# Optimization experiments

Measured on AMD Instinct MI355X. Metric: run time of the kernel, lower is better.

The kernel has to match this reference:

```python
import jax, jax.numpy as jnp
import numpy as np

EPS = 1e-5
BATCH = 2
VOX_H = 8  # grid resolution at depth - stages = 3


def conv_bn_relu(x, neigh, W, gamma, beta):
    # octree sparse conv: gather 27 neighbors per node, then GEMM
    N = neigh.shape[0]
    g = x[neigh].reshape(N, -1)              # [N, 27*Cin]
    y = g @ W                                # [N, Cout]
    mean = jnp.mean(y, axis=0)
    var = jnp.var(y, axis=0)
    y = (y - mean) * jax.lax.rsqrt(var + EPS) * gamma + beta
    return jax.nn.relu(y)


def octree_max_pool(x):
    # max over 8 sibling children -> parent node
    return x.reshape(-1, 8, x.shape[-1]).max(axis=1)


def setup_inputs() -> dict:
    key = jax.random.key(0)
    ks = jax.random.split(key, 8)
    N6, N5, N4, N3 = 524288, 65536, 8192, 1024
    inp = {
        "data": jax.random.normal(ks[0], (N6, 4), jnp.float32),
        "W0": jax.random.normal(ks[1], (108, 16), jnp.float32) * 0.1,
        "g0": jnp.ones((16,), jnp.float32),
        "b0": jnp.zeros((16,), jnp.float32),
        "W1": jax.random.normal(ks[2], (432, 32), jnp.float32) * 0.05,
        "g1": jnp.ones((32,), jnp.float32),
        "b1": jnp.zeros((32,), jnp.float32),
        "W2": jax.random.normal(ks[3], (864, 64), jnp.float32) * 0.05,
        "g2": jnp.ones((64,), jnp.float32),
        "b2": jnp.zeros((64,), jnp.float32),
        "neigh0": jax.random.randint(ks[4], (N6, 27), 0, N6, jnp.int32),
        "neigh1": jax.random.randint(ks[5], (N5, 27), 0, N5, jnp.int32),
        "neigh2": jax.random.randint(ks[6], (N4, 27), 0, N4, jnp.int32),
        "vox_idx": jnp.arange(N3, dtype=jnp.int32),
        "depth": 6,
    }
    return inp


def reference(data, W0, g0, b0, W1, g1, b1, W2, g2, b2,
              neigh0, neigh1, neigh2, vox_idx, depth):
    x = conv_bn_relu(data, neigh0, W0, g0, b0)
    x = octree_max_pool(x)
    x = conv_bn_relu(x, neigh1, W1, g1, b1)
    x = octree_max_pool(x)
    x = conv_bn_relu(x, neigh2, W2, g2, b2)
    x = octree_max_pool(x)                   # [N3, 64]
    # octree2voxel: scatter node features into dense grid per batch sample
    C = x.shape[-1]
    vox = jnp.zeros((BATCH * VOX_H ** 3, C), x.dtype).at[vox_idx].set(x)
    vox = vox.reshape(BATCH, VOX_H, VOX_H, VOX_H, C)
    return vox.transpose(0, 4, 1, 2, 3)      # [B, C, H, H, H]
```

## Files before the change

kernel.cpp:

```cpp
#include <hip/hip_runtime.h>

#define BN_EPS 1e-5f
#define NBUF 64

typedef float        f32x4 __attribute__((ext_vector_type(4)));
typedef float        f32x2 __attribute__((ext_vector_type(2)));
typedef unsigned int u32x2 __attribute__((ext_vector_type(2)));
typedef unsigned int u32x4 __attribute__((ext_vector_type(4)));

__device__ inline unsigned pack_bf16(float a, float b) {
    unsigned ua = __float_as_uint(a);
    unsigned ub = __float_as_uint(b);
    ua = (ua + 0x7fffu + ((ua >> 16) & 1u)) >> 16;
    ub = (ub + 0x7fffu + ((ub >> 16) & 1u)) >> 16;
    return ua | (ub << 16);
}
__device__ inline float bf_lo(unsigned u) { return __uint_as_float(u << 16); }
__device__ inline float bf_hi(unsigned u) { return __uint_as_float(u & 0xffff0000u); }

__global__ void __launch_bounds__(256) cast_bf16_kernel(
    const f32x4* __restrict__ in, u32x2* __restrict__ out, int n4)
{
    const int t = blockIdx.x * 256 + threadIdx.x;
    if (t >= n4) return;
    const f32x4 v = in[t];
    u32x2 r;
    r.x = pack_bf16(v.x, v.y);
    r.y = pack_bf16(v.z, v.w);
    out[t] = r;
}

__global__ void __launch_bounds__(256) conv0_kernel(
    const unsigned long long* __restrict__ xb, const int* __restrict__ neigh,
    const float* __restrict__ W, float* __restrict__ y,
    float* __restrict__ stats)
{
    __shared__ int   idxlds[256 * 27];
    __shared__ float Wlds[27 * 4 * 16];

    for (int i = threadIdx.x; i < 27 * 4 * 16; i += 256) Wlds[i] = W[i];
    {
        const size_t base = (size_t)blockIdx.x * (256 * 27);
        for (int i = threadIdx.x; i < 256 * 27; i += 256)
            idxlds[i] = neigh[base + i];
    }
    __syncthreads();

    const int node = blockIdx.x * 256 + threadIdx.x;

    unsigned long long xr[27];
#pragma unroll
    for (int j = 0; j < 27; ++j) {
        const int nb = idxlds[threadIdx.x * 27 + j];
        xr[j] = __hip_atomic_load(xb + nb, __ATOMIC_RELAXED,
                                  __HIP_MEMORY_SCOPE_AGENT);
    }

    float acc[16];
#pragma unroll
    for (int c = 0; c < 16; ++c) acc[c] = 0.f;

#pragma unroll
    for (int j = 0; j < 27; ++j) {
        const unsigned lo = (unsigned)xr[j];
        const unsigned hi = (unsigned)(xr[j] >> 32);
        float xv[4];
        xv[0] = bf_lo(lo); xv[1] = bf_hi(lo);
        xv[2] = bf_lo(hi); xv[3] = bf_hi(hi);
#pragma unroll
        for (int kk = 0; kk < 4; ++kk) {
            const f32x4* wv = (const f32x4*)&Wlds[(j * 4 + kk) * 16];
#pragma unroll
            for (int c4 = 0; c4 < 4; ++c4) {
                const f32x4 w = wv[c4];
                acc[c4 * 4 + 0] = fmaf(xv[kk], w.x, acc[c4 * 4 + 0]);
                acc[c4 * 4 + 1] = fmaf(xv[kk], w.y, acc[c4 * 4 + 1]);
                acc[c4 * 4 + 2] = fmaf(xv[kk], w.z, acc[c4 * 4 + 2]);
                acc[c4 * 4 + 3] = fmaf(xv[kk], w.w, acc[c4 * 4 + 3]);
            }
        }
    }

    f32x4* yr = (f32x4*)(y + (size_t)node * 16);
#pragma unroll
    for (int c4 = 0; c4 < 4; ++c4) {
        f32x4 v = { acc[c4 * 4 + 0], acc[c4 * 4 + 1], acc[c4 * 4 + 2], acc[c4 * 4 + 3] };
        __builtin_nontemporal_store(v, yr + c4);
    }

    float* buf = stats + (blockIdx.x & (NBUF - 1)) * (2 * 16);
#pragma unroll
    for (int c = 0; c < 16; ++c) {
        float v = acc[c];
        float q = v * v;
#pragma unroll
        for (int off = 32; off > 0; off >>= 1) {
            v += __shfl_xor(v, off, 64);
            q += __shfl_xor(q, off, 64);
        }
        if ((threadIdx.x & 63) == 0) {
            atomicAdd(&buf[c], v);
            atomicAdd(&buf[16 + c], q);
        }
    }
}

__global__ void __launch_bounds__(256) conv1_kernel(
    const u32x4* __restrict__ xb, const int* __restrict__ neigh,
    const float* __restrict__ W, float* __restrict__ y,
    float* __restrict__ stats)
{
    __shared__ float Wlds[27 * 16 * 16];
    const int cobase = blockIdx.y * 16;

    for (int i = threadIdx.x; i < 27 * 16 * 16; i += 256) {
        int k = i >> 4, c = i & 15;
        Wlds[i] = W[k * 32 + cobase + c];
    }
    __syncthreads();

    const int node = blockIdx.x * 256 + threadIdx.x;
    const int* nrow = neigh + (size_t)node * 27;

    int idx[27];
#pragma unroll
    for (int j = 0; j < 27; ++j) idx[j] = nrow[j];

    float acc[16];
#pragma unroll
    for (int c = 0; c < 16; ++c) acc[c] = 0.f;

#pragma unroll 1
    for (int g = 0; g < 27; g += 3) {
        u32x4 xa[3], xc[3];
#pragma unroll
        for (int u = 0; u < 3; ++u) {
            const size_t r = (size_t)idx[g + u] * 2;
            xa[u] = xb[r];
            xc[u] = xb[r + 1];
        }
#pragma unroll
        for (int u = 0; u < 3; ++u) {
            const int j = g + u;
            float xv[16];
            xv[0]  = bf_lo(xa[u].x); xv[1]  = bf_hi(xa[u].x);
            xv[2]  = bf_lo(xa[u].y); xv[3]  = bf_hi(xa[u].y);
            xv[4]  = bf_lo(xa[u].z); xv[5]  = bf_hi(xa[u].z);
            xv[6]  = bf_lo(xa[u].w); xv[7]  = bf_hi(xa[u].w);
            xv[8]  = bf_lo(xc[u].x); xv[9]  = bf_hi(xc[u].x);
            xv[10] = bf_lo(xc[u].y); xv[11] = bf_hi(xc[u].y);
            xv[12] = bf_lo(xc[u].z); xv[13] = bf_hi(xc[u].z);
            xv[14] = bf_lo(xc[u].w); xv[15] = bf_hi(xc[u].w);
#pragma unroll
            for (int k = 0; k < 16; ++k) {
                const f32x4* wv = (const f32x4*)&Wlds[(j * 16 + k) * 16];
#pragma unroll
                for (int c4 = 0; c4 < 4; ++c4) {
                    const f32x4 w = wv[c4];
                    acc[c4 * 4 + 0] = fmaf(xv[k], w.x, acc[c4 * 4 + 0]);
                    acc[c4 * 4 + 1] = fmaf(xv[k], w.y, acc[c4 * 4 + 1]);
                    acc[c4 * 4 + 2] = fmaf(xv[k], w.z, acc[c4 * 4 + 2]);
                    acc[c4 * 4 + 3] = fmaf(xv[k], w.w, acc[c4 * 4 + 3]);
                }
            }
        }
    }

    f32x4* yr = (f32x4*)(y + (size_t)node * 32 + cobase);
#pragma unroll
    for (int c4 = 0; c4 < 4; ++c4) {
        f32x4 v = { acc[c4 * 4 + 0], acc[c4 * 4 + 1], acc[c4 * 4 + 2], acc[c4 * 4 + 3] };
        __builtin_nontemporal_store(v, yr + c4);
    }

    float* buf = stats + (blockIdx.x & (NBUF - 1)) * (2 * 32);
#pragma unroll
    for (int c = 0; c < 16; ++c) {
        float v = acc[c];
        float q = v * v;
#pragma unroll
        for (int off = 32; off > 0; off >>= 1) {
            v += __shfl_xor(v, off, 64);
            q += __shfl_xor(q, off, 64);
        }
        if ((threadIdx.x & 63) == 0) {
            atomicAdd(&buf[cobase + c], v);
            atomicAdd(&buf[32 + cobase + c], q);
        }
    }
}

__global__ void __launch_bounds__(256) conv2_kernel(
    const u32x4* __restrict__ xb, const int* __restrict__ neigh,
    const float* __restrict__ W, float* __restrict__ y,
    float* __restrict__ stats)
{
    __shared__ int idxlds[16 * 27];
    const int nbase = blockIdx.x * 16;
    for (int i = threadIdx.x; i < 16 * 27; i += 256) {
        int n = i / 27, j = i - n * 27;
        idxlds[i] = neigh[(size_t)(nbase + n) * 27 + j];
    }
    __syncthreads();

    const int ln = threadIdx.x >> 4;
    const int c4 = threadIdx.x & 15;
    const int node = nbase + ln;

    f32x4 acc = { 0.f, 0.f, 0.f, 0.f };

#pragma unroll 1
    for (int j = 0; j < 27; ++j) {
        const int nb = idxlds[ln * 27 + j];
        const u32x4* xr = xb + (size_t)nb * 4;
        u32x4 xq[4];
#pragma unroll
        for (int q = 0; q < 4; ++q) xq[q] = xr[q];
#pragma unroll
        for (int q = 0; q < 4; ++q) {
            float xv[8];
            xv[0] = bf_lo(xq[q].x); xv[1] = bf_hi(xq[q].x);
            xv[2] = bf_lo(xq[q].y); xv[3] = bf_hi(xq[q].y);
            xv[4] = bf_lo(xq[q].z); xv[5] = bf_hi(xq[q].z);
            xv[6] = bf_lo(xq[q].w); xv[7] = bf_hi(xq[q].w);
#pragma unroll
            for (int h = 0; h < 8; ++h) {
                const int k = q * 8 + h;
                const f32x4 w = *(const f32x4*)(W + ((size_t)j * 32 + k) * 64 + c4 * 4);
                acc.x = fmaf(xv[h], w.x, acc.x);
                acc.y = fmaf(xv[h], w.y, acc.y);
                acc.z = fmaf(xv[h], w.z, acc.z);
                acc.w = fmaf(xv[h], w.w, acc.w);
            }
        }
    }

    __builtin_nontemporal_store(acc, (f32x4*)(y + (size_t)node * 64 + c4 * 4));

    float sx = acc.x, sy = acc.y, sz = acc.z, sw = acc.w;
    float qx = acc.x * acc.x, qy = acc.y * acc.y, qz = acc.z * acc.z, qw = acc.w * acc.w;
#pragma unroll
    for (int off = 16; off <= 32; off <<= 1) {
        sx += __shfl_xor(sx, off, 64);  sy += __shfl_xor(sy, off, 64);
        sz += __shfl_xor(sz, off, 64);  sw += __shfl_xor(sw, off, 64);
        qx += __shfl_xor(qx, off, 64);  qy += __shfl_xor(qy, off, 64);
        qz += __shfl_xor(qz, off, 64);  qw += __shfl_xor(qw, off, 64);
    }
    if ((threadIdx.x & 63) < 16) {
        float* buf = stats + (blockIdx.x & (NBUF - 1)) * (2 * 64);
        atomicAdd(&buf[c4 * 4 + 0], sx);
        atomicAdd(&buf[c4 * 4 + 1], sy);
        atomicAdd(&buf[c4 * 4 + 2], sz);
        atomicAdd(&buf[c4 * 4 + 3], sw);
        atomicAdd(&buf[64 + c4 * 4 + 0], qx);
        atomicAdd(&buf[64 + c4 * 4 + 1], qy);
        atomicAdd(&buf[64 + c4 * 4 + 2], qz);
        atomicAdd(&buf[64 + c4 * 4 + 3], qw);
    }
}

template<int COUT, bool BF16OUT>
__global__ void __launch_bounds__(256) pool_fin_kernel(
    const float* __restrict__ y, const float* __restrict__ stats,
    const float* __restrict__ gamma, const float* __restrict__ beta,
    void* __restrict__ xout, float invN, int total2)
{
    __shared__ float ss[2 * COUT];
    if (threadIdx.x < COUT) {
        const int c = threadIdx.x;
        float s = 0.f, q = 0.f;
        for (int b = 0; b < NBUF; ++b) {
            s += stats[b * 2 * COUT + c];
            q += stats[b * 2 * COUT + COUT + c];
        }
        const float mean = s * invN;
        const float var  = fmaf(-mean, mean, q * invN);
        const float sc   = gamma[c] * rsqrtf(var + BN_EPS);
        ss[c]        = sc;
        ss[COUT + c] = fmaf(-mean, sc, beta[c]);
    }
    __syncthreads();

    const int t = blockIdx.x * 256 + threadIdx.x;
    if (t >= total2) return;
    const int p  = t / (COUT / 2);
    const int c2 = (t % (COUT / 2)) * 2;
    const float sc0 = ss[c2],     sh0 = ss[COUT + c2];
    const float sc1 = ss[c2 + 1], sh1 = ss[COUT + c2 + 1];
    const float* yr = y + (size_t)p * 8 * COUT + c2;
    float m0 = -3.4e38f, m1 = -3.4e38f;
#pragma unroll
    for (int i = 0; i < 8; ++i) {
        const f32x2 v = __builtin_nontemporal_load((const f32x2*)(yr + i * COUT));
        m0 = fmaxf(m0, fmaf(v.x, sc0, sh0));
        m1 = fmaxf(m1, fmaf(v.y, sc1, sh1));
    }
    m0 = fmaxf(m0, 0.f);
    m1 = fmaxf(m1, 0.f);
    if (BF16OUT) {
        ((unsigned*)xout)[t] = pack_bf16(m0, m1);
    } else {
        f32x2 r = { m0, m1 };
        ((f32x2*)xout)[t] = r;
    }
}

__global__ void __launch_bounds__(256) scatter_kernel(
    const float* __restrict__ x3, const int* __restrict__ vox,
    float* __restrict__ out)
{
    const int t = blockIdx.x * 256 + threadIdx.x;
    const int n = t >> 6, c = t & 63;
    const int r = vox[n];
    out[((r >> 9) << 15) + (c << 9) + (r & 511)] = x3[t];
}

extern "C" void kernel_launch(void* const* d_in, const int* in_sizes, int n_in,
                              void* d_out, int out_size, void* d_ws, size_t ws_size,
                              hipStream_t stream)
{
    const float* data = (const float*)d_in[0];
    const float* W0   = (const float*)d_in[1];
    const float* g0   = (const float*)d_in[2];
    const float* b0   = (const float*)d_in[3];
    const float* W1   = (const float*)d_in[4];
    const float* g1   = (const float*)d_in[5];
    const float* b1   = (const float*)d_in[6];
    const float* W2   = (const float*)d_in[7];
    const float* g2   = (const float*)d_in[8];
    const float* b2   = (const float*)d_in[9];
    const int* neigh0 = (const int*)d_in[10];
    const int* neigh1 = (const int*)d_in[11];
    const int* neigh2 = (const int*)d_in[12];
    const int* vox    = (const int*)d_in[13];

    const int N6 = 524288, N5 = 65536, N4 = 8192, N3 = 1024;

    float* ws = (float*)d_ws;
    const size_t off_y0  = 0;
    const size_t off_xb1 = off_y0 + (size_t)N6 * 16;
    const size_t off_y1  = off_xb1 + (size_t)N5 * 8;
    const size_t off_xb0 = off_y1;
    const size_t off_xb2 = off_y1 + (size_t)N5 * 32;
    const size_t off_y2  = off_xb2 + (size_t)N4 * 16;
    const size_t off_x3  = off_y2 + (size_t)N4 * 64;
    const size_t off_st0 = off_x3 + (size_t)N3 * 64;
    const size_t off_st1 = off_st0 + NBUF * 2 * 16;
    const size_t off_st2 = off_st1 + NBUF * 2 * 32;

    (void)hipMemsetAsync(ws + off_st0, 0, (size_t)(NBUF * 2 * (16 + 32 + 64)) * sizeof(float), stream);

    cast_bf16_kernel<<<N6 / 256, 256, 0, stream>>>(
        (const f32x4*)data, (u32x2*)(ws + off_xb0), N6);
    conv0_kernel<<<N6 / 256, 256, 0, stream>>>(
        (const unsigned long long*)(ws + off_xb0), neigh0, W0, ws + off_y0, ws + off_st0);
    pool_fin_kernel<16, true><<<(N5 * 8) / 256, 256, 0, stream>>>(
        ws + off_y0, ws + off_st0, g0, b0, ws + off_xb1, 1.f / N6, N5 * 8);

    conv1_kernel<<<dim3(N5 / 256, 2), 256, 0, stream>>>(
        (const u32x4*)(ws + off_xb1), neigh1, W1, ws + off_y1, ws + off_st1);
    pool_fin_kernel<32, true><<<(N4 * 16) / 256, 256, 0, stream>>>(
        ws + off_y1, ws + off_st1, g1, b1, ws + off_xb2, 1.f / N5, N4 * 16);

    conv2_kernel<<<N4 / 16, 256, 0, stream>>>(
        (const u32x4*)(ws + off_xb2), neigh2, W2, ws + off_y2, ws + off_st2);
    pool_fin_kernel<64, false><<<(N3 * 32) / 256, 256, 0, stream>>>(
        ws + off_y2, ws + off_st2, g2, b2, ws + off_x3, 1.f / N4, N3 * 32);

    (void)hipMemsetAsync(d_out, 0, (size_t)out_size * sizeof(float), stream);
    scatter_kernel<<<(N3 * 64) / 256, 256, 0, stream>>>(ws + off_x3, vox, (float*)d_out);
}
```

Baseline: 249.5 us.

## Restructure conv0 to cooperative LDS gather and fuse final pool with scatter

conv0 now gathers the 27 neighbor bf16 rows for 128 nodes into shared memory cooperatively, with all threads issuing loads in a flat pattern instead of each thread issuing 27 dependent loads. Four threads then split the 16 output channels per node, with two nodes per thread, and read weights from global/constant cache instead of LDS. The stats reduction is adjusted to match. Separately, the last BN+pool kernel is fused with the voxel scatter, which removes one launch and the x3 round trip. This trades more blocks and a different register footprint for better memory-level parallelism in the gather.

```diff
diff --git a/kernel.cpp b/kernel.cpp
--- a/kernel.cpp
+++ b/kernel.cpp
@@ -31,76 +31,69 @@
 }
 
 __global__ void __launch_bounds__(256) conv0_kernel(
-    const unsigned long long* __restrict__ xb, const int* __restrict__ neigh,
+    const u32x2* __restrict__ xb, const int* __restrict__ neigh,
     const float* __restrict__ W, float* __restrict__ y,
     float* __restrict__ stats)
 {
-    __shared__ int   idxlds[256 * 27];
-    __shared__ float Wlds[27 * 4 * 16];
-
-    for (int i = threadIdx.x; i < 27 * 4 * 16; i += 256) Wlds[i] = W[i];
+    __shared__ u32x2 xs[128 * 27];
+
+    const int nbase = blockIdx.x * 128;
     {
-        const size_t base = (size_t)blockIdx.x * (256 * 27);
-        for (int i = threadIdx.x; i < 256 * 27; i += 256)
-            idxlds[i] = neigh[base + i];
-    }
-    __syncthreads();
-
-    const int node = blockIdx.x * 256 + threadIdx.x;
-
-    unsigned long long xr[27];
+        const int* nb = neigh + (size_t)nbase * 27;
+#pragma unroll
+        for (int i = 0; i < 14; ++i) {
+            const int r = threadIdx.x + 256 * i;
+            if (r < 128 * 27) xs[r] = xb[nb[r]];
+        }
+    }
+    __syncthreads();
+
+    const int ln = threadIdx.x >> 2;
+    const int c4 = threadIdx.x & 3;
+
+    float a0[4] = {0.f, 0.f, 0.f, 0.f};
+    float a1[4] = {0.f, 0.f, 0.f, 0.f};
+
 #pragma unroll
     for (int j = 0; j < 27; ++j) {
-        const int nb = idxlds[threadIdx.x * 27 + j];
-        xr[j] = __hip_atomic_load(xb + nb, __ATOMIC_RELAXED,
-                                  __HIP_MEMORY_SCOPE_AGENT);
-    }
-
-    float acc[16];
-#pragma unroll
-    for (int c = 0; c < 16; ++c) acc[c] = 0.f;
-
-#pragma unroll
-    for (int j = 0; j < 27; ++j) {
-        const unsigned lo = (unsigned)xr[j];
-        const unsigned hi = (unsigned)(xr[j] >> 32);
-        float xv[4];
-        xv[0] = bf_lo(lo); xv[1] = bf_hi(lo);
-        xv[2] = bf_lo(hi); xv[3] = bf_hi(hi);
+        const u32x2 rA = xs[ln * 27 + j];
+        const u32x2 rB = xs[(ln + 64) * 27 + j];
+        float xA[4], xB[4];
+        xA[0] = bf_lo(rA.x); xA[1] = bf_hi(rA.x);
+        xA[2] = bf_lo(rA.y); xA[3] = bf_hi(rA.y);
+        xB[0] = bf_lo(rB.x); xB[1] = bf_hi(rB.x);
+        xB[2] = bf_lo(rB.y); xB[3] = bf_hi(rB.y);
 #pragma unroll
         for (int kk = 0; kk < 4; ++kk) {
-            const f32x4* wv = (const f32x4*)&Wlds[(j * 4 + kk) * 16];
-#pragma unroll
-            for (int c4 = 0; c4 < 4; ++c4) {
-                const f32x4 w = wv[c4];
-                acc[c4 * 4 + 0] = fmaf(xv[kk], w.x, acc[c4 * 4 + 0]);
-                acc[c4 * 4 + 1] = fmaf(xv[kk], w.y, acc[c4 * 4 + 1]);
-                acc[c4 * 4 + 2] = fmaf(xv[kk], w.z, acc[c4 * 4 + 2]);
-                acc[c4 * 4 + 3] = fmaf(xv[kk], w.w, acc[c4 * 4 + 3]);
+            const f32x4 w = *(const f32x4*)(W + ((j * 4 + kk) << 4) + (c4 << 2));
+#pragma unroll
+            for (int i = 0; i < 4; ++i) {
+                a0[i] = fmaf(xA[kk], w[i], a0[i]);
+                a1[i] = fmaf(xB[kk], w[i], a1[i]);
             }
         }
     }
 
-    f32x4* yr = (f32x4*)(y + (size_t)node * 16);
-#pragma unroll
-    for (int c4 = 0; c4 < 4; ++c4) {
-        f32x4 v = { acc[c4 * 4 + 0], acc[c4 * 4 + 1], acc[c4 * 4 + 2], acc[c4 * 4 + 3] };
-        __builtin_nontemporal_store(v, yr + c4);
+    {
+        f32x4 v0 = { a0[0], a0[1], a0[2], a0[3] };
+        f32x4 v1 = { a1[0], a1[1], a1[2], a1[3] };
+        __builtin_nontemporal_store(v0, (f32x4*)(y + (size_t)(nbase + ln) * 16 + (c4 << 2)));
+        __builtin_nontemporal_store(v1, (f32x4*)(y + (size_t)(nbase + 64 + ln) * 16 + (c4 << 2)));
     }
 
     float* buf = stats + (blockIdx.x & (NBUF - 1)) * (2 * 16);
 #pragma unroll
-    for (int c = 0; c < 16; ++c) {
-        float v = acc[c];
-        float q = v * v;
-#pragma unroll
-        for (int off = 32; off > 0; off >>= 1) {
+    for (int i = 0; i < 4; ++i) {
+        float v = a0[i] + a1[i];
+        float q = a0[i] * a0[i] + a1[i] * a1[i];
+#pragma unroll
+        for (int off = 4; off <= 32; off <<= 1) {
             v += __shfl_xor(v, off, 64);
             q += __shfl_xor(q, off, 64);
         }
-        if ((threadIdx.x & 63) == 0) {
-            atomicAdd(&buf[c], v);
-            atomicAdd(&buf[16 + c], q);
+        if ((threadIdx.x & 63) < 4) {
+            atomicAdd(&buf[(c4 << 2) + i], v);
+            atomicAdd(&buf[16 + (c4 << 2) + i], q);
         }
     }
 }
@@ -305,14 +298,47 @@
     }
 }
 
-__global__ void __launch_bounds__(256) scatter_kernel(
-    const float* __restrict__ x3, const int* __restrict__ vox,
-    float* __restrict__ out)
-{
+__global__ void __launch_bounds__(256) pool_fin2_scatter_kernel(
+    const float* __restrict__ y, const float* __restrict__ stats,
+    const float* __restrict__ gamma, const float* __restrict__ beta,
+    const int* __restrict__ vox, float* __restrict__ out, float invN)
+{
+    __shared__ float ss[128];
+    if (threadIdx.x < 64) {
+        const int c = threadIdx.x;
+        float s = 0.f, q = 0.f;
+        for (int b = 0; b < NBUF; ++b) {
+            s += stats[b * 128 + c];
+            q += stats[b * 128 + 64 + c];
+        }
+        const float mean = s * invN;
+        const float var  = fmaf(-mean, mean, q * invN);
+        const float sc   = gamma[c] * rsqrtf(var + BN_EPS);
+        ss[c]      = sc;
+        ss[64 + c] = fmaf(-mean, sc, beta[c]);
+    }
+    __syncthreads();
+
     const int t = blockIdx.x * 256 + threadIdx.x;
-    const int n = t >> 6, c = t & 63;
-    const int r = vox[n];
-    out[((r >> 9) << 15) + (c << 9) + (r & 511)] = x3[t];
+    const int p  = t >> 5;
+    const int c2 = (t & 31) * 2;
+    const float sc0 = ss[c2],     sh0 = ss[64 + c2];
+    const float sc1 = ss[c2 + 1], sh1 = ss[64 + c2 + 1];
+    const float* yr = y + (size_t)p * 8 * 64 + c2;
+    float m0 = -3.4e38f, m1 = -3.4e38f;
+#pragma unroll
+    for (int i = 0; i < 8; ++i) {
+        const f32x2 v = __builtin_nontemporal_load((const f32x2*)(yr + i * 64));
+        m0 = fmaxf(m0, fmaf(v.x, sc0, sh0));
+        m1 = fmaxf(m1, fmaf(v.y, sc1, sh1));
+    }
+    m0 = fmaxf(m0, 0.f);
+    m1 = fmaxf(m1, 0.f);
+
+    const int r = vox[p];
+    const int base = ((r >> 9) << 15) + (r & 511);
+    out[base + (c2 << 9)]       = m0;
+    out[base + ((c2 + 1) << 9)] = m1;
 }
 
 extern "C" void kernel_launch(void* const* d_in, const int* in_sizes, int n_in,
@@ -343,8 +369,7 @@
     const size_t off_xb0 = off_y1;
     const size_t off_xb2 = off_y1 + (size_t)N5 * 32;
     const size_t off_y2  = off_xb2 + (size_t)N4 * 16;
-    const size_t off_x3  = off_y2 + (size_t)N4 * 64;
-    const size_t off_st0 = off_x3 + (size_t)N3 * 64;
+    const size_t off_st0 = off_y2 + (size_t)N4 * 64;
     const size_t off_st1 = off_st0 + NBUF * 2 * 16;
     const size_t off_st2 = off_st1 + NBUF * 2 * 32;
 
@@ -352,8 +377,8 @@
 
     cast_bf16_kernel<<<N6 / 256, 256, 0, stream>>>(
         (const f32x4*)data, (u32x2*)(ws + off_xb0), N6);
-    conv0_kernel<<<N6 / 256, 256, 0, stream>>>(
-        (const unsigned long long*)(ws + off_xb0), neigh0, W0, ws + off_y0, ws + off_st0);
+    conv0_kernel<<<N6 / 128, 256, 0, stream>>>(
+        (const u32x2*)(ws + off_xb0), neigh0, W0, ws + off_y0, ws + off_st0);
     pool_fin_kernel<16, true><<<(N5 * 8) / 256, 256, 0, stream>>>(
         ws + off_y0, ws + off_st0, g0, b0, ws + off_xb1, 1.f / N6, N5 * 8);
 
@@ -364,9 +389,7 @@
 
     conv2_kernel<<<N4 / 16, 256, 0, stream>>>(
         (const u32x4*)(ws + off_xb2), neigh2, W2, ws + off_y2, ws + off_st2);
-    pool_fin_kernel<64, false><<<(N3 * 32) / 256, 256, 0, stream>>>(
-        ws + off_y2, ws + off_st2, g2, b2, ws + off_x3, 1.f / N4, N3 * 32);
-
     (void)hipMemsetAsync(d_out, 0, (size_t)out_size * sizeof(float), stream);
-    scatter_kernel<<<(N3 * 64) / 256, 256, 0, stream>>>(ws + off_x3, vox, (float*)d_out);
-}
+    pool_fin2_scatter_kernel<<<(N3 * 32) / 256, 256, 0, stream>>>(
+        ws + off_y2, ws + off_st2, g2, b2, vox, (float*)d_out, 1.f / N4);
+}
```

Result: no change. 249.2 us (-0.1%).

## Split conv1 nodes across lane pairs and fuse final pool with voxel scatter

Applied to the files above, without the earlier changes.

conv1 now assigns each node to two adjacent lanes, each computing 16 of the 32 output channels. Each lane loads half of every gathered bf16 row and exchanges it with its partner through a shuffle, so the row is gathered once rather than once per channel-half block. Neighbor indices and the full weight matrix are staged in LDS. The last pool/BN/ReLU kernel is fused with the voxel scatter, which removes one launch and the intermediate x3 buffer, at the cost of more LDS and extra shuffle and select instructions in conv1.

```diff
diff --git a/kernel.cpp b/kernel.cpp
--- a/kernel.cpp
+++ b/kernel.cpp
@@ -110,21 +110,21 @@
     const float* __restrict__ W, float* __restrict__ y,
     float* __restrict__ stats)
 {
-    __shared__ float Wlds[27 * 16 * 16];
-    const int cobase = blockIdx.y * 16;
-
-    for (int i = threadIdx.x; i < 27 * 16 * 16; i += 256) {
-        int k = i >> 4, c = i & 15;
-        Wlds[i] = W[k * 32 + cobase + c];
+    __shared__ float Wlds[27 * 16 * 32];
+    __shared__ int   idxlds[128 * 27];
+
+    for (int i = threadIdx.x; i < 27 * 16 * 32; i += 256) Wlds[i] = W[i];
+    {
+        const size_t base = (size_t)blockIdx.x * (128 * 27);
+        for (int i = threadIdx.x; i < 128 * 27; i += 256)
+            idxlds[i] = neigh[base + i];
     }
     __syncthreads();
 
-    const int node = blockIdx.x * 256 + threadIdx.x;
-    const int* nrow = neigh + (size_t)node * 27;
-
-    int idx[27];
-#pragma unroll
-    for (int j = 0; j < 27; ++j) idx[j] = nrow[j];
+    const int nl   = threadIdx.x >> 1;
+    const int half = threadIdx.x & 1;
+    const int node = blockIdx.x * 128 + nl;
+    const int cobase = half << 4;
 
     float acc[16];
 #pragma unroll
@@ -132,28 +132,40 @@
 
 #pragma unroll 1
     for (int g = 0; g < 27; g += 3) {
-        u32x4 xa[3], xc[3];
+        u32x4 mine[3];
 #pragma unroll
         for (int u = 0; u < 3; ++u) {
-            const size_t r = (size_t)idx[g + u] * 2;
-            xa[u] = xb[r];
-            xc[u] = xb[r + 1];
+            const size_t r = (size_t)idxlds[nl * 27 + g + u] * 2 + half;
+            mine[u] = xb[r];
         }
 #pragma unroll
         for (int u = 0; u < 3; ++u) {
             const int j = g + u;
+            u32x4 oth;
+            oth.x = (unsigned)__shfl_xor((int)mine[u].x, 1, 64);
+            oth.y = (unsigned)__shfl_xor((int)mine[u].y, 1, 64);
+            oth.z = (unsigned)__shfl_xor((int)mine[u].z, 1, 64);
+            oth.w = (unsigned)__shfl_xor((int)mine[u].w, 1, 64);
+            const unsigned a0 = half ? oth.x : mine[u].x;
+            const unsigned a1 = half ? oth.y : mine[u].y;
+            const unsigned a2 = half ? oth.z : mine[u].z;
+            const unsigned a3 = half ? oth.w : mine[u].w;
+            const unsigned b0 = half ? mine[u].x : oth.x;
+            const unsigned b1 = half ? mine[u].y : oth.y;
+            const unsigned b2 = half ? mine[u].z : oth.z;
+            const unsigned b3 = half ? mine[u].w : oth.w;
             float xv[16];
-            xv[0]  = bf_lo(xa[u].x); xv[1]  = bf_hi(xa[u].x);
-            xv[2]  = bf_lo(xa[u].y); xv[3]  = bf_hi(xa[u].y);
-            xv[4]  = bf_lo(xa[u].z); xv[5]  = bf_hi(xa[u].z);
-            xv[6]  = bf_lo(xa[u].w); xv[7]  = bf_hi(xa[u].w);
-            xv[8]  = bf_lo(xc[u].x); xv[9]  = bf_hi(xc[u].x);
-            xv[10] = bf_lo(xc[u].y); xv[11] = bf_hi(xc[u].y);
-            xv[12] = bf_lo(xc[u].z); xv[13] = bf_hi(xc[u].z);
-            xv[14] = bf_lo(xc[u].w); xv[15] = bf_hi(xc[u].w);
+            xv[0]  = bf_lo(a0); xv[1]  = bf_hi(a0);
+            xv[2]  = bf_lo(a1); xv[3]  = bf_hi(a1);
+            xv[4]  = bf_lo(a2); xv[5]  = bf_hi(a2);
+            xv[6]  = bf_lo(a3); xv[7]  = bf_hi(a3);
+            xv[8]  = bf_lo(b0); xv[9]  = bf_hi(b0);
+            xv[10] = bf_lo(b1); xv[11] = bf_hi(b1);
+            xv[12] = bf_lo(b2); xv[13] = bf_hi(b2);
+            xv[14] = bf_lo(b3); xv[15] = bf_hi(b3);
 #pragma unroll
             for (int k = 0; k < 16; ++k) {
-                const f32x4* wv = (const f32x4*)&Wlds[(j * 16 + k) * 16];
+                const f32x4* wv = (const f32x4*)&Wlds[(j * 16 + k) * 32 + cobase];
 #pragma unroll
                 for (int c4 = 0; c4 < 4; ++c4) {
                     const f32x4 w = wv[c4];
@@ -179,11 +191,11 @@
         float v = acc[c];
         float q = v * v;
 #pragma unroll
-        for (int off = 32; off > 0; off >>= 1) {
+        for (int off = 2; off <= 32; off <<= 1) {
             v += __shfl_xor(v, off, 64);
             q += __shfl_xor(q, off, 64);
         }
-        if ((threadIdx.x & 63) == 0) {
+        if ((threadIdx.x & 63) < 2) {
             atomicAdd(&buf[cobase + c], v);
             atomicAdd(&buf[32 + cobase + c], q);
         }
@@ -305,14 +317,47 @@
     }
 }
 
-__global__ void __launch_bounds__(256) scatter_kernel(
-    const float* __restrict__ x3, const int* __restrict__ vox,
-    float* __restrict__ out)
-{
+__global__ void __launch_bounds__(256) pool_fin2_scatter_kernel(
+    const float* __restrict__ y, const float* __restrict__ stats,
+    const float* __restrict__ gamma, const float* __restrict__ beta,
+    const int* __restrict__ vox, float* __restrict__ out, float invN)
+{
+    __shared__ float ss[128];
+    if (threadIdx.x < 64) {
+        const int c = threadIdx.x;
+        float s = 0.f, q = 0.f;
+        for (int b = 0; b < NBUF; ++b) {
+            s += stats[b * 128 + c];
+            q += stats[b * 128 + 64 + c];
+        }
+        const float mean = s * invN;
+        const float var  = fmaf(-mean, mean, q * invN);
+        const float sc   = gamma[c] * rsqrtf(var + BN_EPS);
+        ss[c]      = sc;
+        ss[64 + c] = fmaf(-mean, sc, beta[c]);
+    }
+    __syncthreads();
+
     const int t = blockIdx.x * 256 + threadIdx.x;
-    const int n = t >> 6, c = t & 63;
-    const int r = vox[n];
-    out[((r >> 9) << 15) + (c << 9) + (r & 511)] = x3[t];
+    const int p  = t >> 5;
+    const int c2 = (t & 31) * 2;
+    const float sc0 = ss[c2],     sh0 = ss[64 + c2];
+    const float sc1 = ss[c2 + 1], sh1 = ss[64 + c2 + 1];
+    const float* yr = y + (size_t)p * 8 * 64 + c2;
+    float m0 = -3.4e38f, m1 = -3.4e38f;
+#pragma unroll
+    for (int i = 0; i < 8; ++i) {
+        const f32x2 v = __builtin_nontemporal_load((const f32x2*)(yr + i * 64));
+        m0 = fmaxf(m0, fmaf(v.x, sc0, sh0));
+        m1 = fmaxf(m1, fmaf(v.y, sc1, sh1));
+    }
+    m0 = fmaxf(m0, 0.f);
+    m1 = fmaxf(m1, 0.f);
+
+    const int r = vox[p];
+    const int base = ((r >> 9) << 15) + (r & 511);
+    out[base + (c2 << 9)]       = m0;
+    out[base + ((c2 + 1) << 9)] = m1;
 }
 
 extern "C" void kernel_launch(void* const* d_in, const int* in_sizes, int n_in,
@@ -343,8 +388,7 @@
     const size_t off_xb0 = off_y1;
     const size_t off_xb2 = off_y1 + (size_t)N5 * 32;
     const size_t off_y2  = off_xb2 + (size_t)N4 * 16;
-    const size_t off_x3  = off_y2 + (size_t)N4 * 64;
-    const size_t off_st0 = off_x3 + (size_t)N3 * 64;
+    const size_t off_st0 = off_y2 + (size_t)N4 * 64;
     const size_t off_st1 = off_st0 + NBUF * 2 * 16;
     const size_t off_st2 = off_st1 + NBUF * 2 * 32;
 
@@ -357,16 +401,14 @@
     pool_fin_kernel<16, true><<<(N5 * 8) / 256, 256, 0, stream>>>(
         ws + off_y0, ws + off_st0, g0, b0, ws + off_xb1, 1.f / N6, N5 * 8);
 
-    conv1_kernel<<<dim3(N5 / 256, 2), 256, 0, stream>>>(
+    conv1_kernel<<<N5 / 128, 256, 0, stream>>>(
         (const u32x4*)(ws + off_xb1), neigh1, W1, ws + off_y1, ws + off_st1);
     pool_fin_kernel<32, true><<<(N4 * 16) / 256, 256, 0, stream>>>(
         ws + off_y1, ws + off_st1, g1, b1, ws + off_xb2, 1.f / N5, N4 * 16);
 
     conv2_kernel<<<N4 / 16, 256, 0, stream>>>(
         (const u32x4*)(ws + off_xb2), neigh2, W2, ws + off_y2, ws + off_st2);
-    pool_fin_kernel<64, false><<<(N3 * 32) / 256, 256, 0, stream>>>(
-        ws + off_y2, ws + off_st2, g2, b2, ws + off_x3, 1.f / N4, N3 * 32);
-
     (void)hipMemsetAsync(d_out, 0, (size_t)out_size * sizeof(float), stream);
-    scatter_kernel<<<(N3 * 64) / 256, 256, 0, stream>>>(ws + off_x3, vox, (float*)d_out);
-}
+    pool_fin2_scatter_kernel<<<(N3 * 32) / 256, 256, 0, stream>>>(
+        ws + off_y2, ws + off_st2, g2, b2, vox, (float*)d_out, 1.f / N4);
+}
```

New measurement: 275.3 us. +10.3%, slower.
